# Optimization experiments

Hardware: AMD Instinct MI355X
Metric: run time of the kernel (lower is better)

Reference implementation:

```python
import jax, jax.numpy as jnp
import numpy as np
import math

MODES = 32
IN_CH = 32
OUT_CH = 32
SIZE = 2048
BATCH = 8
FILTER_STRENGTH = 4.0
MAX_AMP = 1.0
AMP_SHARP = 1.0
POLE_OFF_SCALE = 0.1
POLE_MIN = 0.1
POLE_MAX = 100.0
CAUSAL_SAFETY = 1.0


def setup_inputs() -> dict:
    key = jax.random.key(0)
    ks = jax.random.split(key, 6)
    # polar-amp init matching the torch module
    fan_in = MODES * IN_CH
    target_amp = math.sqrt(2.0 / fan_in)
    target_sig = max(0.01, min(0.99, target_amp / MAX_AMP))
    init_bias = math.log(target_sig / (1.0 - target_sig)) / AMP_SHARP
    init_scale = 1.0 / math.sqrt(IN_CH * OUT_CH * MODES)
    return {
        "x": jax.random.normal(ks[0], (BATCH, IN_CH, SIZE), jnp.float32),
        "c_star": jax.random.uniform(ks[1], (BATCH,), jnp.float32),
        "dt_star": jnp.full((1,), 0.5, jnp.float32),
        "dx_star": jnp.full((1,), 1.0 / SIZE, jnp.float32),
        "weight_log_amp": init_bias + jax.random.normal(ks[2], (MODES, IN_CH, OUT_CH), jnp.float32) * init_scale,
        "weight_phase": jax.random.normal(ks[3], (MODES, IN_CH, OUT_CH), jnp.float32),
        "log_poles": jnp.linspace(math.log(1.0), math.log(50.0), MODES, dtype=jnp.float32),
        "pole_w": jax.random.normal(ks[4], (IN_CH, MODES), jnp.float32) * math.sqrt(1.0 / IN_CH),
        "pole_b": jnp.zeros((MODES,), jnp.float32),
    }


def _forward(x, weight_log_amp, weight_phase, log_poles, pole_w, pole_b, c_star, dt_star, dx_star):
    size = x.shape[-1]
    # data-dependent pole shift: mean over batch and grid -> [C]
    x_mean = x.mean(axis=(0, 2))
    pole_offsets = jnp.tanh(x_mean @ pole_w + pole_b)           # [K]
    poles = jax.nn.softplus(log_poles + POLE_OFF_SCALE * pole_offsets)
    poles = jnp.clip(poles, POLE_MIN, POLE_MAX)                  # [K]
    # polar weight parameterisation
    weight_amp = MAX_AMP * jax.nn.sigmoid(AMP_SHARP * weight_log_amp)
    weights = weight_amp * jnp.cos(weight_phase)                 # [K,I,O]
    # exponential spectral filter over poles
    k_norm = jnp.arange(MODES, dtype=jnp.float32) / max(MODES - 1, 1)
    pole_filter = jnp.exp(-FILTER_STRENGTH * k_norm ** 2)       # [K]
    # pairwise distances on [0,1] grid
    coords = jnp.linspace(0.0, 1.0, size, dtype=jnp.float32)
    dist = jnp.abs(coords[None, :] - coords[:, None])            # [S,S]
    # data-dependent causal mask: c_eff = safety * max(c_star)
    max_dist_norm = CAUSAL_SAFETY * jnp.max(c_star) * dt_star[0]
    causal = (dist <= max_dist_norm).astype(jnp.float32)         # [S,S]
    # Laplace kernels per pole: exp(-s_k |x-y|), masked, row-normalised
    raw = jnp.exp(-poles[:, None, None] * dist[None]) * causal[None]   # [K,S,S]
    row_norms = jnp.clip(jnp.sum(raw, axis=-1, keepdims=True), 1e-8, None)
    kernels = raw / jax.lax.stop_gradient(row_norms)
    kernels = kernels * pole_filter[:, None, None]
    # contract over source grid j, then mode-wise channel mixing
    out = jnp.einsum('bcs,kts,kio->bot', x, kernels, weights)    # [B,O,S]
    return out


def reference(x, c_star, dt_star, dx_star, weight_log_amp, weight_phase, log_poles, pole_w, pole_b):
    return _forward(x, weight_log_amp, weight_phase, log_poles, pole_w, pole_b, c_star, dt_star, dx_star)
```

## Files before the change

kernel.cpp:

```cpp
#include <hip/hip_runtime.h>
#include <math.h>

#define SM1 2047.0f

#define WS_WSUM  128
#define WS_PART  1312
#define WS_PXS   2048
#define WS_SCALE 133120
#define WS_YF    198656
#define WS_YB    722944

__global__ __launch_bounds__(256) void k1(const float* __restrict__ x,
                                          const float* __restrict__ wla,
                                          const float* __restrict__ wph,
                                          float* __restrict__ ws) {
    int blk = blockIdx.x, tid = threadIdx.x;
    if (blk >= 64) {
        int k = ((blk - 64) << 3) + (tid >> 5);
        int o = tid & 31;
        float a = 0.f;
#pragma unroll 4
        for (int c = 0; c < 32; ++c) {
            int e = (((k << 5) + c) << 5) + o;
            a += cosf(wph[e]) / (1.0f + expf(-wla[e]));
        }
        ws[WS_WSUM + (k << 5) + o] = a;
        return;
    }
    int b = blk >> 3, q = blk & 7;
    const float4* x4 = (const float4*)x + ((size_t)(((b << 5) + (q << 2))) << 9);
    __shared__ float pr[8][4];
    float4 ae = make_float4(0.f, 0.f, 0.f, 0.f);
    float4 ao = make_float4(0.f, 0.f, 0.f, 0.f);
    int wid = tid >> 6;
#pragma unroll
    for (int it = 0; it < 8; ++it) {
        float4 v = x4[(it << 8) + tid];
        float pc = (v.x + v.y) + (v.z + v.w);
        if (it & 1) { ao.x += v.x; ao.y += v.y; ao.z += v.z; ao.w += v.w; }
        else        { ae.x += v.x; ae.y += v.y; ae.z += v.z; ae.w += v.w; }
        for (int off = 32; off; off >>= 1) pc += __shfl_xor(pc, off, 64);
        if ((tid & 63) == 0) pr[it][wid] = pc;
    }
    float4* pxs4 = (float4*)(ws + WS_PXS) + ((size_t)(((b << 3) + q)) << 9);
    pxs4[tid] = ae;
    pxs4[256 + tid] = ao;
    __syncthreads();
    if (tid < 4) {
        float m = 0.f;
#pragma unroll
        for (int w = 0; w < 4; ++w) m += pr[(tid << 1)][w] + pr[(tid << 1) + 1][w];
        ws[WS_PART + (blk << 2) + tid] = m;
    }
}

__global__ __launch_bounds__(256) void k2(const float* __restrict__ c_star,
                                          const float* __restrict__ dt,
                                          const float* __restrict__ lp,
                                          const float* __restrict__ pw,
                                          const float* __restrict__ pb,
                                          float* __restrict__ ws) {
    __shared__ float xr[2048];
    __shared__ float carr[32][9];
    __shared__ float xm[32], cP[32], cD[32], cDW1[32], cDL[32], cPF[32], cIDEN[32];
    __shared__ int cWsh;
    int tid = threadIdx.x, blk = blockIdx.x;
    if (tid < 32) {
        float m = 0.f;
#pragma unroll
        for (int b = 0; b < 8; ++b) m += ws[WS_PART + (b << 5) + tid];
        xm[tid] = m * (1.0f / 16384.0f);
    }
    __syncthreads();
    if (tid < 32) {
        int k = tid;
        float mc = c_star[0];
        for (int b2 = 1; b2 < 8; ++b2) mc = fmaxf(mc, c_star[b2]);
        float mdn = mc * dt[0];
        int W = (int)(mdn * SM1);
        while (W + 1 <= 2047 && (float)(W + 1) / SM1 <= mdn) ++W;
        while (W > 0 && (float)W / SM1 > mdn) --W;
        W = min(max(W, 0), 2047);
        if (k == 0) cWsh = W;
        float accp = pb[k];
        for (int c = 0; c < 32; ++c) accp += xm[c] * pw[(c << 5) + k];
        float z = lp[k] + 0.1f * tanhf(accp);
        float p = log1pf(expf(z));
        p = fminf(fmaxf(p, 0.1f), 100.0f);
        float d = expf(-p / SM1);
        cP[k]   = p;
        cD[k]   = d;
        cDW1[k] = expf(-p * (float)(W + 1) / SM1);
        cDL[k]  = expf(-p * 64.0f / SM1);
        float kn = (float)k / 31.0f;
        cPF[k]  = expf(-4.0f * kn * kn);
        cIDEN[k] = d / (-expm1f(-p / SM1));
    }
    __syncthreads();
    int W = cWsh;

    if (blk >= 64) {
        int k = blk - 64;
        float p = cP[k], iden = cIDEN[k], pf = cPF[k];
        float rs = 1.0f / SM1;
#pragma unroll
        for (int j = 0; j < 8; ++j) {
            int t = (j << 8) + tid;
            int n1 = min(W, t), n2 = min(W, 2047 - t);
            float g1 = -iden * expm1f(-p * (float)n1 * rs);
            float g2 = -iden * expm1f(-p * (float)n2 * rs);
            ws[WS_SCALE + (k << 11) + t] = pf / (1.0f + g1 + g2);
        }
        return;
    }
    int b = blk >> 3, dir = (blk >> 2) & 1, kq = blk & 3;
#pragma unroll
    for (int j = 0; j < 8; ++j) {
        int idx = (j << 8) + tid;
        float s8 = 0.f;
#pragma unroll
        for (int q = 0; q < 8; ++q) s8 += ws[WS_PXS + (((b << 3) + q) << 11) + idx];
        xr[idx] = s8;
    }
    __syncthreads();
    int chunk = tid >> 3, kk = tid & 7;
    int k = (kq << 3) + kk;
    float d = cD[k], dw1 = cDW1[k], dL = cDL[k];
    float st = 0.f;
    if (dir == 0) {
        int t0 = chunk << 6;
#pragma unroll
        for (int i = 0; i < 64; ++i) {
            int t = t0 + i;
            float u = xr[t];
            int tl = t - W - 1;
            if (tl >= 0) u = fmaf(-dw1, xr[tl], u);
            st = fmaf(d, st, u);
        }
    } else {
        int t1 = (chunk << 6) + 63;
#pragma unroll
        for (int i = 0; i < 64; ++i) {
            int t = t1 - i;
            float u = xr[t];
            int th = t + W + 1;
            if (th <= 2047) u = fmaf(-dw1, xr[th], u);
            st = fmaf(d, st, u);
        }
    }
    int sidx = (dir == 0) ? chunk : 31 - chunk;
    carr[sidx][kk] = st;
    float m = dL, cur = st;
    for (int off = 1; off < 32; off <<= 1) {
        __syncthreads();
        float prev = (sidx >= off) ? carr[sidx - off][kk] : 0.f;
        __syncthreads();
        cur = fmaf(m, prev, cur);
        carr[sidx][kk] = cur;
        m = m * m;
    }
    __syncthreads();
    float cin = (sidx == 0) ? 0.f : carr[sidx - 1][kk];
    float* yo = ws + ((dir == 0) ? WS_YF : WS_YB) + (((size_t)((b << 5) + k)) << 11);
    float4 v4;
    st = cin;
    if (dir == 0) {
        int t0 = chunk << 6;
#pragma unroll
        for (int i = 0; i < 64; ++i) {
            int t = t0 + i;
            float u = xr[t];
            int tl = t - W - 1;
            if (tl >= 0) u = fmaf(-dw1, xr[tl], u);
            st = fmaf(d, st, u);
            int ph = i & 3;
            if (ph == 0) v4.x = st; else if (ph == 1) v4.y = st;
            else if (ph == 2) v4.z = st;
            else { v4.w = st; *(float4*)(yo + (t & ~3)) = v4; }
        }
    } else {
        int t1 = (chunk << 6) + 63;
#pragma unroll
        for (int i = 0; i < 64; ++i) {
            int t = t1 - i;
            float u = xr[t];
            int th = t + W + 1;
            if (th <= 2047) u = fmaf(-dw1, xr[th], u);
            st = fmaf(d, st, u);
            float val = st - xr[t];
            int ph = t & 3;
            if (ph == 3) v4.w = val; else if (ph == 2) v4.z = val;
            else if (ph == 1) v4.y = val;
            else { v4.x = val; *(float4*)(yo + t) = v4; }
        }
    }
}

__global__ __launch_bounds__(1024) void k3(const float* __restrict__ ws,
                                           float* __restrict__ out) {
    __shared__ float wl[1024];
    __shared__ float yt[32 * 33];
    int tid = threadIdx.x;
    int b = blockIdx.x >> 6;
    int t0 = (blockIdx.x & 63) << 5;
    wl[tid] = ws[WS_WSUM + tid];
    {
        int k = tid >> 5, tt = tid & 31;
        size_t yi = (((size_t)((b << 5) + k)) << 11) + t0 + tt;
        float sc = ws[WS_SCALE + (k << 11) + t0 + tt];
        yt[tt * 33 + k] = (ws[WS_YF + yi] + ws[WS_YB + yi]) * sc;
    }
    __syncthreads();
    {
        int o = tid >> 5, tt = tid & 31;
        float acc = 0.f;
#pragma unroll
        for (int kk = 0; kk < 32; ++kk)
            acc = fmaf(yt[tt * 33 + kk], wl[(kk << 5) + o], acc);
        out[((size_t)((b << 5) + o) << 11) + t0 + tt] = acc;
    }
}

extern "C" void kernel_launch(void* const* d_in, const int* in_sizes, int n_in,
                              void* d_out, int out_size, void* d_ws, size_t ws_size,
                              hipStream_t stream) {
    const float* x      = (const float*)d_in[0];
    const float* c_star = (const float*)d_in[1];
    const float* dt     = (const float*)d_in[2];
    const float* wla    = (const float*)d_in[4];
    const float* wph    = (const float*)d_in[5];
    const float* lp     = (const float*)d_in[6];
    const float* pw     = (const float*)d_in[7];
    const float* pb     = (const float*)d_in[8];
    float* out = (float*)d_out;
    float* ws  = (float*)d_ws;

    k1<<<68,  256,  0, stream>>>(x, wla, wph, ws);
    k2<<<96,  256,  0, stream>>>(c_star, dt, lp, pw, pb, ws);
    k3<<<512, 1024, 0, stream>>>(ws, out);
}
```

Measured before the change: 31.20 us.

## Merge forward/backward scans in one block, sum in shared memory, scale computed in k3

```diff
diff --git a/kernel.cpp b/kernel.cpp
--- a/kernel.cpp
+++ b/kernel.cpp
@@ -3,12 +3,14 @@
 
 #define SM1 2047.0f
 
+#define WS_P     0
+#define WS_IDEN  32
+#define WS_PF    64
+#define WS_WIDX  96
 #define WS_WSUM  128
 #define WS_PART  1312
 #define WS_PXS   2048
-#define WS_SCALE 133120
-#define WS_YF    198656
-#define WS_YB    722944
+#define WS_Y     133120
 
 __global__ __launch_bounds__(256) void k1(const float* __restrict__ x,
                                           const float* __restrict__ wla,
@@ -54,21 +56,30 @@
     }
 }
 
-__global__ __launch_bounds__(256) void k2(const float* __restrict__ c_star,
+__global__ __launch_bounds__(512) void k2(const float* __restrict__ c_star,
                                           const float* __restrict__ dt,
                                           const float* __restrict__ lp,
                                           const float* __restrict__ pw,
                                           const float* __restrict__ pb,
                                           float* __restrict__ ws) {
     __shared__ float xr[2048];
-    __shared__ float carr[32][9];
+    __shared__ float yt[32][8][65];
+    __shared__ float carr[2][32][9];
     __shared__ float xm[32], cP[32], cD[32], cDW1[32], cDL[32], cPF[32], cIDEN[32];
     __shared__ int cWsh;
     int tid = threadIdx.x, blk = blockIdx.x;
+    int b = blk >> 2, kq = blk & 3;
+
+    for (int i = tid; i < 2048; i += 512) {
+        float s8 = 0.f;
+#pragma unroll
+        for (int q = 0; q < 8; ++q) s8 += ws[WS_PXS + (((b << 3) + q) << 11) + i];
+        xr[i] = s8;
+    }
     if (tid < 32) {
         float m = 0.f;
 #pragma unroll
-        for (int b = 0; b < 8; ++b) m += ws[WS_PART + (b << 5) + tid];
+        for (int bb = 0; bb < 8; ++bb) m += ws[WS_PART + (bb << 5) + tid];
         xm[tid] = m * (1.0f / 16384.0f);
     }
     __syncthreads();
@@ -95,37 +106,20 @@
         float kn = (float)k / 31.0f;
         cPF[k]  = expf(-4.0f * kn * kn);
         cIDEN[k] = d / (-expm1f(-p / SM1));
-    }
-    __syncthreads();
-    int W = cWsh;
-
-    if (blk >= 64) {
-        int k = blk - 64;
-        float p = cP[k], iden = cIDEN[k], pf = cPF[k];
-        float rs = 1.0f / SM1;
-#pragma unroll
-        for (int j = 0; j < 8; ++j) {
-            int t = (j << 8) + tid;
-            int n1 = min(W, t), n2 = min(W, 2047 - t);
-            float g1 = -iden * expm1f(-p * (float)n1 * rs);
-            float g2 = -iden * expm1f(-p * (float)n2 * rs);
-            ws[WS_SCALE + (k << 11) + t] = pf / (1.0f + g1 + g2);
-        }
-        return;
-    }
-    int b = blk >> 3, dir = (blk >> 2) & 1, kq = blk & 3;
-#pragma unroll
-    for (int j = 0; j < 8; ++j) {
-        int idx = (j << 8) + tid;
-        float s8 = 0.f;
-#pragma unroll
-        for (int q = 0; q < 8; ++q) s8 += ws[WS_PXS + (((b << 3) + q) << 11) + idx];
-        xr[idx] = s8;
-    }
-    __syncthreads();
-    int chunk = tid >> 3, kk = tid & 7;
+        if (blk == 0) {
+            ws[WS_P + k]    = p;
+            ws[WS_IDEN + k] = cIDEN[k];
+            ws[WS_PF + k]   = cPF[k];
+            if (k == 0) ((int*)ws)[WS_WIDX] = W;
+        }
+    }
+    __syncthreads();
+
+    int dir = tid >> 8, lid = tid & 255;
+    int chunk = lid >> 3, kk = lid & 7;
     int k = (kq << 3) + kk;
     float d = cD[k], dw1 = cDW1[k], dL = cDL[k];
+    int W = cWsh;
     float st = 0.f;
     if (dir == 0) {
         int t0 = chunk << 6;
@@ -149,22 +143,21 @@
         }
     }
     int sidx = (dir == 0) ? chunk : 31 - chunk;
-    carr[sidx][kk] = st;
+    carr[dir][sidx][kk] = st;
     float m = dL, cur = st;
     for (int off = 1; off < 32; off <<= 1) {
         __syncthreads();
-        float prev = (sidx >= off) ? carr[sidx - off][kk] : 0.f;
+        float prev = (sidx >= off) ? carr[dir][sidx - off][kk] : 0.f;
         __syncthreads();
         cur = fmaf(m, prev, cur);
-        carr[sidx][kk] = cur;
+        carr[dir][sidx][kk] = cur;
         m = m * m;
     }
     __syncthreads();
-    float cin = (sidx == 0) ? 0.f : carr[sidx - 1][kk];
-    float* yo = ws + ((dir == 0) ? WS_YF : WS_YB) + (((size_t)((b << 5) + k)) << 11);
-    float4 v4;
-    st = cin;
+    float cin = (sidx == 0) ? 0.f : carr[dir][sidx - 1][kk];
+
     if (dir == 0) {
+        st = cin;
         int t0 = chunk << 6;
 #pragma unroll
         for (int i = 0; i < 64; ++i) {
@@ -173,12 +166,12 @@
             int tl = t - W - 1;
             if (tl >= 0) u = fmaf(-dw1, xr[tl], u);
             st = fmaf(d, st, u);
-            int ph = i & 3;
-            if (ph == 0) v4.x = st; else if (ph == 1) v4.y = st;
-            else if (ph == 2) v4.z = st;
-            else { v4.w = st; *(float4*)(yo + (t & ~3)) = v4; }
-        }
-    } else {
+            yt[chunk][kk][i] = st;
+        }
+    }
+    __syncthreads();
+    if (dir == 1) {
+        st = cin;
         int t1 = (chunk << 6) + 63;
 #pragma unroll
         for (int i = 0; i < 64; ++i) {
@@ -187,28 +180,37 @@
             int th = t + W + 1;
             if (th <= 2047) u = fmaf(-dw1, xr[th], u);
             st = fmaf(d, st, u);
-            float val = st - xr[t];
-            int ph = t & 3;
-            if (ph == 3) v4.w = val; else if (ph == 2) v4.z = val;
-            else if (ph == 1) v4.y = val;
-            else { v4.x = val; *(float4*)(yo + t) = v4; }
-        }
+            yt[chunk][kk][63 - i] += st - xr[t];
+        }
+    }
+    __syncthreads();
+    {
+        int w = tid >> 6, l = tid & 63;
+        float* yg = ws + WS_Y + (((size_t)((b << 5) + (kq << 3) + w)) << 11);
+#pragma unroll
+        for (int j = 0; j < 32; ++j)
+            yg[(j << 6) + l] = yt[j][w][l];
     }
 }
 
 __global__ __launch_bounds__(1024) void k3(const float* __restrict__ ws,
                                            float* __restrict__ out) {
     __shared__ float wl[1024];
-    __shared__ float yt[32 * 33];
+    __shared__ float yts[32 * 33];
     int tid = threadIdx.x;
     int b = blockIdx.x >> 6;
     int t0 = (blockIdx.x & 63) << 5;
     wl[tid] = ws[WS_WSUM + tid];
     {
         int k = tid >> 5, tt = tid & 31;
-        size_t yi = (((size_t)((b << 5) + k)) << 11) + t0 + tt;
-        float sc = ws[WS_SCALE + (k << 11) + t0 + tt];
-        yt[tt * 33 + k] = (ws[WS_YF + yi] + ws[WS_YB + yi]) * sc;
+        int t = t0 + tt;
+        float p = ws[WS_P + k], iden = ws[WS_IDEN + k], pf = ws[WS_PF + k];
+        int W = ((const int*)ws)[WS_WIDX];
+        int n1 = min(W, t), n2 = min(W, 2047 - t);
+        float g1 = -iden * expm1f(-p * (float)n1 * (1.0f / SM1));
+        float g2 = -iden * expm1f(-p * (float)n2 * (1.0f / SM1));
+        float sc = pf / (1.0f + g1 + g2);
+        yts[tt * 33 + k] = ws[WS_Y + (((size_t)((b << 5) + k)) << 11) + t] * sc;
     }
     __syncthreads();
     {
@@ -216,7 +218,7 @@
         float acc = 0.f;
 #pragma unroll
         for (int kk = 0; kk < 32; ++kk)
-            acc = fmaf(yt[tt * 33 + kk], wl[(kk << 5) + o], acc);
+            acc = fmaf(yts[tt * 33 + kk], wl[(kk << 5) + o], acc);
         out[((size_t)((b << 5) + o) << 11) + t0 + tt] = acc;
     }
 }
@@ -236,6 +238,6 @@
     float* ws  = (float*)d_ws;
 
     k1<<<68,  256,  0, stream>>>(x, wla, wph, ws);
-    k2<<<96,  256,  0, stream>>>(c_star, dt, lp, pw, pb, ws);
+    k2<<<32,  512,  0, stream>>>(c_star, dt, lp, pw, pb, ws);
     k3<<<512, 1024, 0, stream>>>(ws, out);
 }
```

After: 36.04 us. 15.5% more time.
